# Kernel optimization log

Measured on AMD Instinct MI355X. Metric: run time of the kernel, lower is better.

## Reference

```python
import jax, jax.numpy as jnp
import numpy as np

DIM = 768
HEADS = 12
HEAD_DIM = 64
TOTAL = HEADS * HEAD_DIM
EPS = 1e-5


def setup_inputs() -> dict:
    key = jax.random.key(0)
    ks = jax.random.split(key, 8)
    B, P = 4, 2048
    x = jax.random.normal(ks[0], (B, P, DIM), dtype=jnp.float32)
    ln_w = jnp.ones((DIM,), jnp.float32)
    ln_b = jnp.zeros((DIM,), jnp.float32)
    s = 1.0 / np.sqrt(DIM)
    Wq = jax.random.normal(ks[1], (DIM, TOTAL), jnp.float32) * s
    Wk = jax.random.normal(ks[2], (DIM, TOTAL), jnp.float32) * s
    Wv = jax.random.normal(ks[3], (DIM, TOTAL), jnp.float32) * s
    bv = jax.random.normal(ks[4], (TOTAL,), jnp.float32) * 0.01
    Wfc = jax.random.normal(ks[5], (TOTAL, DIM), jnp.float32) * (1.0 / np.sqrt(TOTAL))
    bfc = jax.random.normal(ks[6], (DIM,), jnp.float32) * 0.01
    return {"x": x, "ln_w": ln_w, "ln_b": ln_b, "Wq": Wq, "Wk": Wk,
            "Wv": Wv, "bv": bv, "Wfc": Wfc, "bfc": bfc}


def _msa(x, ln_w, ln_b, Wq, Wk, Wv, bv, Wfc, bfc):
    # pre-norm LayerNorm
    mu = jnp.mean(x, axis=-1, keepdims=True)
    var = jnp.mean(jnp.square(x - mu), axis=-1, keepdims=True)
    xn = (x - mu) * jax.lax.rsqrt(var + EPS) * ln_w + ln_b
    B, P, _ = xn.shape
    # separate Q/K/V projections; reshape b p (h d) -> b h p d
    q = (xn @ Wq).reshape(B, P, HEADS, HEAD_DIM).transpose(0, 2, 1, 3)
    k = (xn @ Wk).reshape(B, P, HEADS, HEAD_DIM).transpose(0, 2, 1, 3)
    v = (xn @ Wv + bv).reshape(B, P, HEADS, HEAD_DIM).transpose(0, 2, 1, 3)
    scale = 1.0 / np.sqrt(HEAD_DIM).astype(np.float32)
    R = jnp.einsum('bhpd,bhqd->bhpq', q, k) * scale  # [B,H,P,P]
    # mask_self: -inf on the diagonal
    diag = jnp.eye(P, dtype=bool)
    R = jnp.where(diag, -jnp.inf, R)
    attn = jax.nn.softmax(R, axis=-1)
    out = jnp.einsum('bhpq,bhqd->bhpd', attn, v)
    out = out.transpose(0, 2, 1, 3).reshape(B, P, TOTAL)  # b h p d -> b p (h d)
    return out @ Wfc + bfc


def reference(x, ln_w, ln_b, Wq, Wk, Wv, bv, Wfc, bfc):
    return _msa(x, ln_w, ln_b, Wq, Wk, Wv, bv, Wfc, bfc)
```

## Files before the change

kernel.cpp:

```cpp
#include <hip/hip_runtime.h>

#define DIM    768
#define HEADS  12
#define HD     64
#define BB     4
#define PP     2048
#define MTOT   8192
#define NQKV   2304
#define QBLK   128

typedef unsigned short bf16s;
typedef short bf16x8 __attribute__((ext_vector_type(8)));
typedef float f32x4  __attribute__((ext_vector_type(4)));

typedef const __attribute__((address_space(1))) unsigned int g_u32;
typedef __attribute__((address_space(3))) unsigned int lds_u32;

__device__ __forceinline__ bf16s f2bf(float f) {
    unsigned int u = __float_as_uint(f);
    unsigned int r = u + 0x7fffu + ((u >> 16) & 1u);
    return (bf16s)(r >> 16);
}
__device__ __forceinline__ float bf2f(bf16s s) {
    return __uint_as_float(((unsigned int)s) << 16);
}
__device__ __forceinline__ float exp2g(float x) {
    return __builtin_amdgcn_exp2f(x);
}
__device__ __forceinline__ unsigned cvt_pk_bf16(float a, float b) {
    unsigned r;
    asm("v_cvt_pk_bf16_f32 %0, %1, %2" : "=v"(r) : "v"(a), "v"(b));
    return r;
}

__global__ __launch_bounds__(256) void ln_kernel(
        const float* __restrict__ x, const float* __restrict__ w,
        const float* __restrict__ b, bf16s* __restrict__ xn) {
    int row = blockIdx.x;
    const float* xr = x + (size_t)row * DIM;
    int t = threadIdx.x;
    float v0 = xr[t], v1 = xr[t + 256], v2 = xr[t + 512];
    float s  = v0 + v1 + v2;
    float ss = v0*v0 + v1*v1 + v2*v2;
    for (int off = 32; off; off >>= 1) {
        s  += __shfl_down(s, off);
        ss += __shfl_down(ss, off);
    }
    __shared__ float red[8];
    int wid = t >> 6, lane = t & 63;
    if (lane == 0) { red[wid] = s; red[4 + wid] = ss; }
    __syncthreads();
    if (t == 0) {
        float S  = red[0] + red[1] + red[2] + red[3];
        float SS = red[4] + red[5] + red[6] + red[7];
        float mean = S * (1.0f / DIM);
        float var  = SS * (1.0f / DIM) - mean * mean;
        red[0] = mean;
        red[1] = rsqrtf(var + 1e-5f);
    }
    __syncthreads();
    float mean = red[0], inv = red[1];
    bf16s* xo = xn + (size_t)row * DIM;
    xo[t]       = f2bf((v0 - mean) * inv * w[t]       + b[t]);
    xo[t + 256] = f2bf((v1 - mean) * inv * w[t + 256] + b[t + 256]);
    xo[t + 512] = f2bf((v2 - mean) * inv * w[t + 512] + b[t + 512]);
}

__global__ __launch_bounds__(256) void transpose_all(
        const float* __restrict__ Wq, const float* __restrict__ Wk,
        const float* __restrict__ Wv, const float* __restrict__ Wfc,
        bf16s* __restrict__ Wqkv_t, bf16s* __restrict__ Wfc_h,
        bf16s* __restrict__ Wfc_l, float sc) {
    int z = blockIdx.z;
    const float* src = (z == 0) ? Wq : (z == 1) ? Wk : (z == 2) ? Wv : Wfc;
    float scale = (z == 0) ? sc : 1.0f;
    __shared__ float tile[32][33];
    int n0 = blockIdx.x * 32, k0 = blockIdx.y * 32;
    int tx = threadIdx.x, ty = threadIdx.y;
    #pragma unroll
    for (int i = 0; i < 4; ++i)
        tile[ty + 8*i][tx] = src[(size_t)(k0 + ty + 8*i) * DIM + n0 + tx];
    __syncthreads();
    #pragma unroll
    for (int i = 0; i < 4; ++i) {
        float v = tile[tx][ty + 8*i] * scale;
        size_t oidx = (size_t)(n0 + ty + 8*i) * DIM + k0 + tx;
        bf16s hi = f2bf(v);
        if (z < 3) {
            Wqkv_t[(size_t)z * DIM * DIM + oidx] = hi;
        } else {
            Wfc_h[oidx] = hi;
            Wfc_l[oidx] = f2bf(v - bf2f(hi));
        }
    }
}

template<int MODE>
__global__ __launch_bounds__(256) void gemm_bt(
        const bf16s* __restrict__ A0, const bf16s* __restrict__ A1,
        const bf16s* __restrict__ B0, const bf16s* __restrict__ B1,
        const float* __restrict__ bias,
        bf16s* __restrict__ Qo, bf16s* __restrict__ Ko, bf16s* __restrict__ Vo,
        float* __restrict__ out) {
    const int BN   = (MODE == 0 ? 128 : 64);
    const int NI   = (MODE == 0 ? 4 : 2);
    const int BISS = (MODE == 0 ? 4 : 2);
    const int NT   = (MODE == 0 ? NQKV / 128 : DIM / 64);
    const int NWG  = (MTOT / 128) * NT;
    int bid = blockIdx.x;
    bid = (bid & 7) * (NWG / 8) + (bid >> 3);
    int nt = bid % NT, mt = bid / NT;
    int m0 = mt * 128, n0 = nt * BN;
    __shared__ bf16s As[128 * 64];
    __shared__ bf16s Bs[BN * 64];
    int t = threadIdx.x;
    int lane = t & 63, w = t >> 6;
    int wr = w >> 1, wc = w & 1;
    int lr = lane & 15, lg = lane >> 4;
    int sflat[4];
    size_t sgoff[4];
    #pragma unroll
    for (int i = 0; i < 4; ++i) {
        int flat = i * 2048 + t * 8;
        int r = flat >> 6, c = flat & 63;
        int csw = (((c >> 3) ^ (r & 7)) << 3);
        sflat[i] = flat;
        sgoff[i] = (size_t)r * DIM + csw;
    }
    const int xorv = (lr & 7) << 3;
    f32x4 acc[4][NI] = {};
    const int KI = (MODE == 0 ? DIM / 64 : 3 * DIM / 64);
    for (int it = 0; it < KI; ++it) {
        int seg = it / (DIM / 64);
        int k0  = (it % (DIM / 64)) * 64;
        const bf16s* Ap = A0;
        const bf16s* Bp = B0;
        if (MODE == 1) {
            Ap = (seg == 2) ? A1 : A0;
            Bp = (seg == 1) ? B1 : B0;
        }
        #pragma unroll
        for (int i = 0; i < 4; ++i)
            __builtin_amdgcn_global_load_lds(
                (g_u32*)(Ap + (size_t)m0 * DIM + k0 + sgoff[i]),
                (lds_u32*)&As[sflat[i]], 16, 0, 0);
        #pragma unroll
        for (int i = 0; i < BISS; ++i)
            __builtin_amdgcn_global_load_lds(
                (g_u32*)(Bp + (size_t)n0 * DIM + k0 + sgoff[i]),
                (lds_u32*)&Bs[sflat[i]], 16, 0, 0);
        __syncthreads();
        #pragma unroll
        for (int kk = 0; kk < 2; ++kk) {
            bf16x8 af[4], bfr[NI];
            #pragma unroll
            for (int i = 0; i < 4; ++i) {
                int arow = wr*64 + i*16 + lr;
                af[i] = *(const bf16x8*)&As[arow*64 + ((kk*32 + lg*8) ^ xorv)];
            }
            #pragma unroll
            for (int i = 0; i < NI; ++i) {
                int brow = wc*(BN/2) + i*16 + lr;
                bfr[i] = *(const bf16x8*)&Bs[brow*64 + ((kk*32 + lg*8) ^ xorv)];
            }
            #pragma unroll
            for (int mi = 0; mi < 4; ++mi)
                #pragma unroll
                for (int ni = 0; ni < NI; ++ni)
                    acc[mi][ni] = __builtin_amdgcn_mfma_f32_16x16x32_bf16(
                        af[mi], bfr[ni], acc[mi][ni], 0, 0, 0);
        }
        __syncthreads();
    }
    if (MODE == 0) {
        #pragma unroll
        for (int mi = 0; mi < 4; ++mi) {
            int m_base = m0 + wr*64 + mi*16 + lg*4;
            int b = m_base >> 11, p = m_base & 2047;
            #pragma unroll
            for (int ni = 0; ni < NI; ++ni) {
                int n = n0 + wc*64 + ni*16 + lr;
                int which = n / DIM, within = n % DIM;
                int hh = within >> 6, d = within & 63;
                if (which == 2) {
                    float bb = bias[within];
                    uint2 pk;
                    pk.x = cvt_pk_bf16(acc[mi][ni][0] + bb, acc[mi][ni][1] + bb);
                    pk.y = cvt_pk_bf16(acc[mi][ni][2] + bb, acc[mi][ni][3] + bb);
                    *(uint2*)&Vo[(((size_t)(b*HEADS + hh))*HD + d)*PP + p] = pk;
                } else {
                    bf16s* dst = (which == 1) ? Ko : Qo;
                    #pragma unroll
                    for (int r = 0; r < 4; ++r)
                        dst[(((size_t)(b*HEADS + hh))*PP + p + r)*HD + d] =
                            f2bf(acc[mi][ni][r]);
                }
            }
        }
    } else {
        #pragma unroll
        for (int mi = 0; mi < 4; ++mi)
            #pragma unroll
            for (int ni = 0; ni < NI; ++ni)
                #pragma unroll
                for (int r = 0; r < 4; ++r) {
                    int m = m0 + wr*64 + mi*16 + lg*4 + r;
                    int n = n0 + wc*32 + ni*16 + lr;
                    out[(size_t)m * DIM + n] = acc[mi][ni][r] + bias[n];
                }
    }
}

__global__ __launch_bounds__(256, 3) void attn_kernel(
        const bf16s* __restrict__ Q, const bf16s* __restrict__ K,
        const bf16s* __restrict__ Vt,
        bf16s* __restrict__ Oh, bf16s* __restrict__ Ol) {
    const int NWG = BB * HEADS * (PP / QBLK);
    int orig = blockIdx.x;
    int wg = (orig & 7) * (NWG / 8) + (orig >> 3);
    int qt  = wg & 15;
    int tmp = wg >> 4;
    int h   = tmp % HEADS;
    int b   = tmp / HEADS;
    const size_t headoff = ((size_t)(b * HEADS + h)) * PP * HD;
    const bf16s* Qh = Q  + headoff;
    const bf16s* Kh = K  + headoff;
    const bf16s* Vh = Vt + headoff;
    __shared__ bf16s Ks[2][64 * 64];
    __shared__ bf16s Vs[2][64 * 64];
    __shared__ bf16s Ps[4][16 * 64];
    int t = threadIdx.x, lane = t & 63, w = t >> 6;
    int lr = lane & 15, lg = lane >> 4;
    int q0  = qt * QBLK;
    int qw0 = q0 + w * 32;
    const int xorv = (lr & 7) << 3;
    bf16x8 qf[2][2];
    #pragma unroll
    for (int u = 0; u < 2; ++u) {
        qf[u][0] = *(const bf16x8*)&Qh[(size_t)(qw0 + 16*u + lr) * HD + lg*8];
        qf[u][1] = *(const bf16x8*)&Qh[(size_t)(qw0 + 16*u + lr) * HD + 32 + lg*8];
    }
    float m_run[2] = {-1e30f, -1e30f};
    float l_run[2] = {0.f, 0.f};
    f32x4 o[2][4] = {};
    int sflat[2];
    size_t skoff[2], svoff[2];
    #pragma unroll
    for (int i = 0; i < 2; ++i) {
        int flat = i * 2048 + t * 8;
        int r = flat >> 6, c = flat & 63;
        int csw = (((c >> 3) ^ (r & 7)) << 3);
        sflat[i] = flat;
        skoff[i] = (size_t)r * HD + csw;
        svoff[i] = (size_t)r * PP + csw;
    }
    #pragma unroll
    for (int i = 0; i < 2; ++i) {
        __builtin_amdgcn_global_load_lds((g_u32*)(Kh + skoff[i]),
                                         (lds_u32*)&Ks[0][sflat[i]], 16, 0, 0);
        __builtin_amdgcn_global_load_lds((g_u32*)(Vh + svoff[i]),
                                         (lds_u32*)&Vs[0][sflat[i]], 16, 0, 0);
    }
    __syncthreads();
    for (int j = 0; j < 32; ++j) {
        int cur = j & 1;
        if (j < 31) {
            #pragma unroll
            for (int i = 0; i < 2; ++i) {
                __builtin_amdgcn_global_load_lds(
                    (g_u32*)(Kh + (size_t)(j+1)*64*HD + skoff[i]),
                    (lds_u32*)&Ks[cur ^ 1][sflat[i]], 16, 0, 0);
                __builtin_amdgcn_global_load_lds(
                    (g_u32*)(Vh + svoff[i] + (j+1)*64),
                    (lds_u32*)&Vs[cur ^ 1][sflat[i]], 16, 0, 0);
            }
        }
        f32x4 s[2][4] = {};
        #pragma unroll
        for (int kk = 0; kk < 2; ++kk) {
            bf16x8 kf[4];
            #pragma unroll
            for (int n = 0; n < 4; ++n)
                kf[n] = *(const bf16x8*)&Ks[cur][(n*16 + lr)*64 + ((kk*32 + lg*8) ^ xorv)];
            #pragma unroll
            for (int u = 0; u < 2; ++u)
                #pragma unroll
                for (int n = 0; n < 4; ++n)
                    s[u][n] = __builtin_amdgcn_mfma_f32_16x16x32_bf16(
                        kf[n], qf[u][kk], s[u][n], 0, 0, 0);
        }
        #pragma unroll
        for (int u = 0; u < 2; ++u) {
            if (((qw0 + 16*u) >> 6) == j) {
                int qrel = qw0 + 16*u + lr - j*64;
                #pragma unroll
                for (int n = 0; n < 4; ++n)
                    #pragma unroll
                    for (int r = 0; r < 4; ++r)
                        if (n*16 + lg*4 + r == qrel) s[u][n][r] = -1e30f;
            }
        }
        bf16x8 vfreg[2][4];
        #pragma unroll
        for (int kk = 0; kk < 2; ++kk)
            #pragma unroll
            for (int nd = 0; nd < 4; ++nd)
                vfreg[kk][nd] = *(const bf16x8*)&Vs[cur][(nd*16 + lr)*64 + ((kk*32 + lg*8) ^ xorv)];
        #pragma unroll
        for (int u = 0; u < 2; ++u) {
            float mt = -1e30f;
            #pragma unroll
            for (int n = 0; n < 4; ++n)
                #pragma unroll
                for (int r = 0; r < 4; ++r) mt = fmaxf(mt, s[u][n][r]);
            mt = fmaxf(mt, __shfl_xor(mt, 16));
            mt = fmaxf(mt, __shfl_xor(mt, 32));
            if (!__all(mt <= m_run[u] + 8.f)) {
                float mn = fmaxf(m_run[u], mt);
                float corr = exp2g(m_run[u] - mn);
                m_run[u] = mn;
                l_run[u] *= corr;
                #pragma unroll
                for (int r = 0; r < 4; ++r) {
                    float cq = __shfl(corr, lg*4 + r);
                    #pragma unroll
                    for (int nd = 0; nd < 4; ++nd) o[u][nd][r] *= cq;
                }
            }
            float rs = 0.f;
            #pragma unroll
            for (int n = 0; n < 4; ++n)
                #pragma unroll
                for (int r = 0; r < 4; ++r) {
                    float p = exp2g(s[u][n][r] - m_run[u]);
                    s[u][n][r] = p;
                    rs += p;
                }
            rs += __shfl_xor(rs, 16);
            rs += __shfl_xor(rs, 32);
            l_run[u] += rs;
            #pragma unroll
            for (int n = 0; n < 4; ++n) {
                uint2 pk;
                pk.x = cvt_pk_bf16(s[u][n][0], s[u][n][1]);
                pk.y = cvt_pk_bf16(s[u][n][2], s[u][n][3]);
                *(uint2*)&Ps[w][lr*64 + ((n*16 + lg*4) ^ xorv)] = pk;
            }
            asm volatile("s_waitcnt lgkmcnt(0)" ::: "memory");
            __builtin_amdgcn_sched_barrier(0);
            #pragma unroll
            for (int kk = 0; kk < 2; ++kk) {
                bf16x8 pf = *(const bf16x8*)&Ps[w][lr*64 + ((kk*32 + lg*8) ^ xorv)];
                #pragma unroll
                for (int nd = 0; nd < 4; ++nd)
                    o[u][nd] = __builtin_amdgcn_mfma_f32_16x16x32_bf16(
                        pf, vfreg[kk][nd], o[u][nd], 0, 0, 0);
            }
        }
        if (j < 31)
            __syncthreads();
    }
    float invl[2][4];
    #pragma unroll
    for (int u = 0; u < 2; ++u)
        #pragma unroll
        for (int r = 0; r < 4; ++r)
            invl[u][r] = 1.0f / __shfl(l_run[u], lg*4 + r);
    #pragma unroll
    for (int u = 0; u < 2; ++u)
        #pragma unroll
        for (int nd = 0; nd < 4; ++nd)
            #pragma unroll
            for (int r = 0; r < 4; ++r) {
                int q = qw0 + 16*u + lg*4 + r;
                int d = nd*16 + lr;
                float v = o[u][nd][r] * invl[u][r];
                size_t idx = ((size_t)b * PP + q) * DIM + h * HD + d;
                bf16s hi = f2bf(v);
                Oh[idx] = hi;
                Ol[idx] = f2bf(v - bf2f(hi));
            }
}

extern "C" void kernel_launch(void* const* d_in, const int* in_sizes, int n_in,
                              void* d_out, int out_size, void* d_ws, size_t ws_size,
                              hipStream_t stream) {
    const float* x    = (const float*)d_in[0];
    const float* ln_w = (const float*)d_in[1];
    const float* ln_b = (const float*)d_in[2];
    const float* Wq   = (const float*)d_in[3];
    const float* Wk   = (const float*)d_in[4];
    const float* Wv   = (const float*)d_in[5];
    const float* bv   = (const float*)d_in[6];
    const float* Wfc  = (const float*)d_in[7];
    const float* bfc  = (const float*)d_in[8];
    float* out = (float*)d_out;

    char* ws = (char*)d_ws;
    size_t off = 0;
    auto alloc = [&](size_t bytes) {
        void* p = ws + off;
        off += (bytes + 255) & ~(size_t)255;
        return p;
    };
    bf16s* xn     = (bf16s*)alloc((size_t)MTOT * DIM * 2);
    bf16s* Wqkv_t = (bf16s*)alloc((size_t)NQKV * DIM * 2);
    bf16s* Wfc_h  = (bf16s*)alloc((size_t)DIM * DIM * 2);
    bf16s* Wfc_l  = (bf16s*)alloc((size_t)DIM * DIM * 2);
    bf16s* Qb     = (bf16s*)alloc((size_t)MTOT * DIM * 2);
    bf16s* Kb     = (bf16s*)alloc((size_t)MTOT * DIM * 2);
    bf16s* Vtg    = (bf16s*)alloc((size_t)MTOT * DIM * 2);
    bf16s* Ah     = (bf16s*)alloc((size_t)MTOT * DIM * 2);
    bf16s* Al     = (bf16s*)alloc((size_t)MTOT * DIM * 2);

    const float SC = 0.125f * 1.44269504f;

    ln_kernel<<<MTOT, 256, 0, stream>>>(x, ln_w, ln_b, xn);

    transpose_all<<<dim3(24, 24, 4), dim3(32, 8), 0, stream>>>(
        Wq, Wk, Wv, Wfc, Wqkv_t, Wfc_h, Wfc_l, SC);

    gemm_bt<0><<<(MTOT / 128) * (NQKV / 128), 256, 0, stream>>>(
        xn, nullptr, Wqkv_t, nullptr, bv, Qb, Kb, Vtg, nullptr);

    attn_kernel<<<BB * HEADS * (PP / QBLK), 256, 0, stream>>>(Qb, Kb, Vtg, Ah, Al);

    gemm_bt<1><<<(MTOT / 128) * (DIM / 64), 256, 0, stream>>>(
        Ah, Al, Wfc_h, Wfc_l, bfc, nullptr, nullptr, nullptr, out);
}
```

Measured before the change: 185.8 us.

## Switch attention to 32x32x16 MFMA and keep P in registers via permlane swap

Rewrites the attention inner loop to use 32x32x16 bf16 MFMA tiles, one 32-query tile per wave, instead of 16x16x32 tiles. The softmax probabilities are repacked in registers with v_permlane32_swap into the A-operand layout for the PV matmul, which removes the per-wave LDS scratch buffer and its store/wait/load round trip. Row max and sum reductions now need only one cross-lane shuffle. The larger accumulators raise register pressure, so launch bounds drop from 3 to 2 blocks per SIMD, which may reduce occupancy.

```diff
diff --git a/kernel.cpp b/kernel.cpp
--- a/kernel.cpp
+++ b/kernel.cpp
@@ -12,6 +12,7 @@
 typedef unsigned short bf16s;
 typedef short bf16x8 __attribute__((ext_vector_type(8)));
 typedef float f32x4  __attribute__((ext_vector_type(4)));
+typedef float f32x16 __attribute__((ext_vector_type(16)));
 
 typedef const __attribute__((address_space(1))) unsigned int g_u32;
 typedef __attribute__((address_space(3))) unsigned int lds_u32;
@@ -211,7 +212,7 @@
     }
 }
 
-__global__ __launch_bounds__(256, 3) void attn_kernel(
+__global__ __launch_bounds__(256, 2) void attn_kernel(
         const bf16s* __restrict__ Q, const bf16s* __restrict__ K,
         const bf16s* __restrict__ Vt,
         bf16s* __restrict__ Oh, bf16s* __restrict__ Ol) {
@@ -228,21 +229,17 @@
     const bf16s* Vh = Vt + headoff;
     __shared__ bf16s Ks[2][64 * 64];
     __shared__ bf16s Vs[2][64 * 64];
-    __shared__ bf16s Ps[4][16 * 64];
     int t = threadIdx.x, lane = t & 63, w = t >> 6;
-    int lr = lane & 15, lg = lane >> 4;
+    int l31 = lane & 31, hi = lane >> 5;
     int q0  = qt * QBLK;
     int qw0 = q0 + w * 32;
-    const int xorv = (lr & 7) << 3;
-    bf16x8 qf[2][2];
-    #pragma unroll
-    for (int u = 0; u < 2; ++u) {
-        qf[u][0] = *(const bf16x8*)&Qh[(size_t)(qw0 + 16*u + lr) * HD + lg*8];
-        qf[u][1] = *(const bf16x8*)&Qh[(size_t)(qw0 + 16*u + lr) * HD + 32 + lg*8];
-    }
-    float m_run[2] = {-1e30f, -1e30f};
-    float l_run[2] = {0.f, 0.f};
-    f32x4 o[2][4] = {};
+    const int xorv = (l31 & 7) << 3;
+    bf16x8 qf[4];
+    #pragma unroll
+    for (int tt = 0; tt < 4; ++tt)
+        qf[tt] = *(const bf16x8*)&Qh[(size_t)(qw0 + l31) * HD + tt*16 + hi*8];
+    float m_run = -1e30f, l_run = 0.f;
+    f32x16 o32[2] = {};
     int sflat[2];
     size_t skoff[2], svoff[2];
     #pragma unroll
@@ -275,111 +272,99 @@
                     (lds_u32*)&Vs[cur ^ 1][sflat[i]], 16, 0, 0);
             }
         }
-        f32x4 s[2][4] = {};
-        #pragma unroll
-        for (int kk = 0; kk < 2; ++kk) {
-            bf16x8 kf[4];
-            #pragma unroll
-            for (int n = 0; n < 4; ++n)
-                kf[n] = *(const bf16x8*)&Ks[cur][(n*16 + lr)*64 + ((kk*32 + lg*8) ^ xorv)];
-            #pragma unroll
-            for (int u = 0; u < 2; ++u)
+        f32x16 s[2] = {};
+        #pragma unroll
+        for (int kt = 0; kt < 2; ++kt) {
+            #pragma unroll
+            for (int tt = 0; tt < 4; ++tt) {
+                bf16x8 kf = *(const bf16x8*)
+                    &Ks[cur][(kt*32 + l31)*64 + ((tt*16 + hi*8) ^ xorv)];
+                s[kt] = __builtin_amdgcn_mfma_f32_32x32x16_bf16(
+                    kf, qf[tt], s[kt], 0, 0, 0);
+            }
+        }
+        if ((qw0 >> 6) == j) {
+            int qrel = (qw0 & 63) + l31;
+            #pragma unroll
+            for (int kt = 0; kt < 2; ++kt)
                 #pragma unroll
-                for (int n = 0; n < 4; ++n)
-                    s[u][n] = __builtin_amdgcn_mfma_f32_16x16x32_bf16(
-                        kf[n], qf[u][kk], s[u][n], 0, 0, 0);
-        }
-        #pragma unroll
-        for (int u = 0; u < 2; ++u) {
-            if (((qw0 + 16*u) >> 6) == j) {
-                int qrel = qw0 + 16*u + lr - j*64;
-                #pragma unroll
-                for (int n = 0; n < 4; ++n)
-                    #pragma unroll
-                    for (int r = 0; r < 4; ++r)
-                        if (n*16 + lg*4 + r == qrel) s[u][n][r] = -1e30f;
-            }
-        }
-        bf16x8 vfreg[2][4];
-        #pragma unroll
-        for (int kk = 0; kk < 2; ++kk)
-            #pragma unroll
-            for (int nd = 0; nd < 4; ++nd)
-                vfreg[kk][nd] = *(const bf16x8*)&Vs[cur][(nd*16 + lr)*64 + ((kk*32 + lg*8) ^ xorv)];
-        #pragma unroll
-        for (int u = 0; u < 2; ++u) {
-            float mt = -1e30f;
-            #pragma unroll
-            for (int n = 0; n < 4; ++n)
-                #pragma unroll
-                for (int r = 0; r < 4; ++r) mt = fmaxf(mt, s[u][n][r]);
-            mt = fmaxf(mt, __shfl_xor(mt, 16));
-            mt = fmaxf(mt, __shfl_xor(mt, 32));
-            if (!__all(mt <= m_run[u] + 8.f)) {
-                float mn = fmaxf(m_run[u], mt);
-                float corr = exp2g(m_run[u] - mn);
-                m_run[u] = mn;
-                l_run[u] *= corr;
-                #pragma unroll
-                for (int r = 0; r < 4; ++r) {
-                    float cq = __shfl(corr, lg*4 + r);
-                    #pragma unroll
-                    for (int nd = 0; nd < 4; ++nd) o[u][nd][r] *= cq;
-                }
-            }
-            float rs = 0.f;
-            #pragma unroll
-            for (int n = 0; n < 4; ++n)
-                #pragma unroll
-                for (int r = 0; r < 4; ++r) {
-                    float p = exp2g(s[u][n][r] - m_run[u]);
-                    s[u][n][r] = p;
-                    rs += p;
-                }
-            rs += __shfl_xor(rs, 16);
-            rs += __shfl_xor(rs, 32);
-            l_run[u] += rs;
-            #pragma unroll
-            for (int n = 0; n < 4; ++n) {
-                uint2 pk;
-                pk.x = cvt_pk_bf16(s[u][n][0], s[u][n][1]);
-                pk.y = cvt_pk_bf16(s[u][n][2], s[u][n][3]);
-                *(uint2*)&Ps[w][lr*64 + ((n*16 + lg*4) ^ xorv)] = pk;
-            }
-            asm volatile("s_waitcnt lgkmcnt(0)" ::: "memory");
-            __builtin_amdgcn_sched_barrier(0);
-            #pragma unroll
-            for (int kk = 0; kk < 2; ++kk) {
-                bf16x8 pf = *(const bf16x8*)&Ps[w][lr*64 + ((kk*32 + lg*8) ^ xorv)];
-                #pragma unroll
-                for (int nd = 0; nd < 4; ++nd)
-                    o[u][nd] = __builtin_amdgcn_mfma_f32_16x16x32_bf16(
-                        pf, vfreg[kk][nd], o[u][nd], 0, 0, 0);
+                for (int r = 0; r < 16; ++r)
+                    if (kt*32 + (r&3) + 8*(r>>2) + 4*hi == qrel)
+                        s[kt][r] = -1e30f;
+        }
+        float t0[8];
+        #pragma unroll
+        for (int i = 0; i < 8; ++i)
+            t0[i] = fmaxf(fmaxf(s[0][2*i], s[0][2*i+1]),
+                          fmaxf(s[1][2*i], s[1][2*i+1]));
+        float t1a = fmaxf(fmaxf(t0[0], t0[1]), fmaxf(t0[2], t0[3]));
+        float t1b = fmaxf(fmaxf(t0[4], t0[5]), fmaxf(t0[6], t0[7]));
+        float mt = fmaxf(t1a, t1b);
+        mt = fmaxf(mt, __shfl_xor(mt, 32));
+        if (!__all(mt <= m_run + 8.f)) {
+            float mn = fmaxf(m_run, mt);
+            float corr = exp2g(m_run - mn);
+            m_run = mn;
+            l_run *= corr;
+            #pragma unroll
+            for (int r = 0; r < 16; ++r) {
+                float cq = __shfl(corr, (r&3) + 8*(r>>2) + 4*hi);
+                o32[0][r] *= cq;
+                o32[1][r] *= cq;
+            }
+        }
+        #pragma unroll
+        for (int kt = 0; kt < 2; ++kt)
+            #pragma unroll
+            for (int r = 0; r < 16; ++r)
+                s[kt][r] = exp2g(s[kt][r] - m_run);
+        float u0[8];
+        #pragma unroll
+        for (int i = 0; i < 8; ++i)
+            u0[i] = (s[0][2*i] + s[0][2*i+1]) + (s[1][2*i] + s[1][2*i+1]);
+        float rs = ((u0[0] + u0[1]) + (u0[2] + u0[3]))
+                 + ((u0[4] + u0[5]) + (u0[6] + u0[7]));
+        rs += __shfl_xor(rs, 32);
+        l_run += rs;
+        #pragma unroll
+        for (int ks = 0; ks < 4; ++ks) {
+            const int kt = ks >> 1, rb = (ks & 1) * 8;
+            unsigned x0 = cvt_pk_bf16(s[kt][rb+0], s[kt][rb+1]);
+            unsigned x1 = cvt_pk_bf16(s[kt][rb+2], s[kt][rb+3]);
+            unsigned y0 = cvt_pk_bf16(s[kt][rb+4], s[kt][rb+5]);
+            unsigned y1 = cvt_pk_bf16(s[kt][rb+6], s[kt][rb+7]);
+            asm("v_permlane32_swap_b32 %0, %1" : "+v"(x0), "+v"(y0));
+            asm("v_permlane32_swap_b32 %0, %1" : "+v"(x1), "+v"(y1));
+            uint4 pw;
+            pw.x = x0; pw.y = x1; pw.z = y0; pw.w = y1;
+            bf16x8 pa = __builtin_bit_cast(bf16x8, pw);
+            #pragma unroll
+            for (int dt = 0; dt < 2; ++dt) {
+                bf16x8 vb = *(const bf16x8*)
+                    &Vs[cur][(dt*32 + l31)*64 + ((ks*16 + hi*8) ^ xorv)];
+                o32[dt] = __builtin_amdgcn_mfma_f32_32x32x16_bf16(
+                    pa, vb, o32[dt], 0, 0, 0);
             }
         }
         if (j < 31)
             __syncthreads();
     }
-    float invl[2][4];
-    #pragma unroll
-    for (int u = 0; u < 2; ++u)
-        #pragma unroll
-        for (int r = 0; r < 4; ++r)
-            invl[u][r] = 1.0f / __shfl(l_run[u], lg*4 + r);
-    #pragma unroll
-    for (int u = 0; u < 2; ++u)
-        #pragma unroll
-        for (int nd = 0; nd < 4; ++nd)
-            #pragma unroll
-            for (int r = 0; r < 4; ++r) {
-                int q = qw0 + 16*u + lg*4 + r;
-                int d = nd*16 + lr;
-                float v = o[u][nd][r] * invl[u][r];
-                size_t idx = ((size_t)b * PP + q) * DIM + h * HD + d;
-                bf16s hi = f2bf(v);
-                Oh[idx] = hi;
-                Ol[idx] = f2bf(v - bf2f(hi));
-            }
+    float inv = 1.0f / l_run;
+    #pragma unroll
+    for (int r = 0; r < 16; ++r) {
+        int cr = (r&3) + 8*(r>>2) + 4*hi;
+        float iv = __shfl(inv, cr);
+        int q = qw0 + cr;
+        #pragma unroll
+        for (int dt = 0; dt < 2; ++dt) {
+            int d = dt*32 + l31;
+            float v = o32[dt][r] * iv;
+            size_t idx = ((size_t)b * PP + q) * DIM + h * HD + d;
+            bf16s hi16 = f2bf(v);
+            Oh[idx] = hi16;
+            Ol[idx] = f2bf(v - bf2f(hi16));
+        }
+    }
 }
 
 extern "C" void kernel_launch(void* const* d_in, const int* in_sizes, int n_in,
```

New measurement: 181.0 us. -2.6%, faster.
